# Kernel optimization log

Hardware: AMD Instinct MI355X
Metric: run time of the kernel (lower is better)

Reference implementation:

```python
import jax, jax.numpy as jnp
import numpy as np

NUM_TIMES = 1024  # times are drawn from [0, 1024), used as fixed segment count
N = 16777216


def setup_inputs() -> dict:
    key = jax.random.key(0)
    k1, k2, k3 = jax.random.split(key, 3)
    outs = jax.random.normal(k1, (N,), dtype=jnp.float32)
    T_E = jax.random.randint(k2, (N,), 0, 2, dtype=jnp.int32)
    T_T = jax.random.randint(k3, (N,), 0, NUM_TIMES, dtype=jnp.int32)
    return {"outs": outs, "T_E": T_E, "T_T": T_T}


def reference(outs, T_E, T_T):
    # E[E > 0] = 1  -> binary event indicator
    E = (T_E > 0).astype(outs.dtype)
    # Y_label_T = |T_T| ; integer times act directly as segment ids
    seg_ids = jnp.abs(T_T)
    Obs = jnp.sum(E)
    # log of running sum of hazards: log(cumsum(exp(yhat)))
    y_hat_cumsum = jnp.log(jnp.cumsum(jnp.exp(outs)))
    # original segment_max initializes accumulator at 0, so it is clipped below at 0;
    # jnp.maximum also neutralizes -inf fill for empty segments (count=0 there anyway)
    seg_max = jnp.maximum(
        jax.ops.segment_max(y_hat_cumsum, seg_ids, num_segments=NUM_TIMES), 0.0
    )
    seg_cnt = jax.ops.segment_sum(E, seg_ids, num_segments=NUM_TIMES)
    loss_s2 = jnp.sum(seg_max * seg_cnt)
    loss_s1 = jnp.sum(outs * E)
    return (loss_s2 - loss_s1) / Obs
```

## Files before the change

### kernel.cpp

```cpp
#include <hip/hip_runtime.h>

#define NUM_SEGS 1024
#define TILE_LOG 10
#define TILE (1 << TILE_LOG)
#define TPB 16
#define CHUNK (TILE * TPB)
#define BLK 256
#define NREP 32

typedef __attribute__((address_space(3))) void lds_void_t;
typedef __attribute__((address_space(1))) const void glb_void_t;

__device__ __forceinline__ void dma16(const void* g, void* l) {
    __builtin_amdgcn_global_load_lds((glb_void_t*)g, (lds_void_t*)l, 16, 0, 0);
}

__device__ __forceinline__ float waveReduceSumF(float v) {
#pragma unroll
    for (int off = 32; off > 0; off >>= 1) v += __shfl_down(v, off, 64);
    return v;
}
__device__ __forceinline__ unsigned waveReduceSumU(unsigned v) {
#pragma unroll
    for (int off = 32; off > 0; off >>= 1) v += __shfl_down(v, off, 64);
    return v;
}
__device__ __forceinline__ double waveReduceSumD(double v) {
#pragma unroll
    for (int off = 32; off > 0; off >>= 1) v += __shfl_down(v, off, 64);
    return v;
}

__global__ void init_kernel(unsigned* __restrict__ cntRep, int* __restrict__ lmaxRep,
                            unsigned* __restrict__ obs, double* __restrict__ loss1,
                            double* __restrict__ loss2, unsigned* __restrict__ counter) {
    const int t = blockIdx.x * blockDim.x + threadIdx.x;
    if (t < NREP * NUM_SEGS) { cntRep[t] = 0u; lmaxRep[t] = -1; }
    if (t == 0) { obs[0] = 0u; loss1[0] = 0.0; loss2[0] = 0.0; counter[0] = 0u; }
}

__global__ __launch_bounds__(BLK) void pass1_kernel(
    const float* __restrict__ outs, const int* __restrict__ te,
    const int* __restrict__ tt, int N,
    float* __restrict__ tile_sums, unsigned* __restrict__ cntRep,
    int* __restrict__ lmaxRep, unsigned* __restrict__ obs,
    double* __restrict__ loss1) {
    __shared__ __align__(16) float bufO[2][TILE];
    __shared__ __align__(16) int bufE[2][TILE];
    __shared__ __align__(16) int bufS[2][TILE];
    __shared__ unsigned hist[NUM_SEGS];
    __shared__ int lmax[NUM_SEGS];
    __shared__ float redF[BLK / 64];
    __shared__ float redF2[BLK / 64];
    __shared__ unsigned redU[BLK / 64];

    for (int t = threadIdx.x; t < NUM_SEGS; t += BLK) { hist[t] = 0u; lmax[t] = -1; }

    const int base = blockIdx.x * CHUNK;
    float sumOE = 0.f;
    unsigned cntE = 0u;
    const int lane = threadIdx.x & 63, wid = threadIdx.x >> 6;

    if (base + CHUNK <= N) {
        const int lofs = wid << 8;
        const int g0 = base + lofs + (lane << 2);
        auto stage = [&](int k, int b) {
            const int ge = g0 + (k << TILE_LOG);
            dma16(outs + ge, &bufO[b][lofs]);
            dma16(te + ge, &bufE[b][lofs]);
            dma16(tt + ge, &bufS[b][lofs]);
        };
        stage(0, 0);
        stage(1, 1);
        const int t4 = threadIdx.x << 2;
#pragma unroll 1
        for (int k = 0; k < TPB; ++k) {
            const int cur = k & 1;
            __syncthreads();
            const float4 o = *reinterpret_cast<const float4*>(&bufO[cur][t4]);
            const int4 ev = *reinterpret_cast<const int4*>(&bufE[cur][t4]);
            const int4 sv = *reinterpret_cast<const int4*>(&bufS[cur][t4]);
            const int gi = base + (k << TILE_LOG) + t4;
            const int s0 = sv.x < 0 ? -sv.x : sv.x;
            const int s1 = sv.y < 0 ? -sv.y : sv.y;
            const int s2 = sv.z < 0 ? -sv.z : sv.z;
            const int s3 = sv.w < 0 ? -sv.w : sv.w;
            lmax[s0] = gi;
            lmax[s1] = gi + 1;
            lmax[s2] = gi + 2;
            lmax[s3] = gi + 3;
            const float se = (__expf(o.x) + __expf(o.y)) + (__expf(o.z) + __expf(o.w));
            if (ev.x > 0) { cntE++; sumOE += o.x; atomicAdd(&hist[s0], 1u); }
            if (ev.y > 0) { cntE++; sumOE += o.y; atomicAdd(&hist[s1], 1u); }
            if (ev.z > 0) { cntE++; sumOE += o.z; atomicAdd(&hist[s2], 1u); }
            if (ev.w > 0) { cntE++; sumOE += o.w; atomicAdd(&hist[s3], 1u); }
            const float w = waveReduceSumF(se);
            if (lane == 0) redF[wid] = w;
            __syncthreads();
            if (threadIdx.x == 0)
                tile_sums[(base >> TILE_LOG) + k] =
                    (redF[0] + redF[1]) + (redF[2] + redF[3]);
            if (k + 2 < TPB) stage(k + 2, cur);
        }
    } else {
        for (int k = 0; k < TPB; ++k) {
            const int tbase = base + (k << TILE_LOG);
            float se = 0.f;
            const int end = (tbase + TILE < N) ? tbase + TILE : N;
            for (int i = tbase + (int)threadIdx.x; i < end; i += BLK) {
                const float o = outs[i];
                const int e = te[i];
                int s = tt[i]; s = s < 0 ? -s : s;
                se += __expf(o);
                lmax[s] = i;
                if (e > 0) { cntE++; sumOE += o; atomicAdd(&hist[s], 1u); }
            }
            const float w = waveReduceSumF(se);
            if (lane == 0) redF[wid] = w;
            __syncthreads();
            if (threadIdx.x == 0 && tbase < N)
                tile_sums[(base >> TILE_LOG) + k] =
                    (redF[0] + redF[1]) + (redF[2] + redF[3]);
            __syncthreads();
        }
    }
    __syncthreads();

    const int rep = (blockIdx.x & (NREP - 1)) << 10;
    for (int t = threadIdx.x; t < NUM_SEGS; t += BLK) {
        const unsigned h = hist[t];
        if (h) atomicAdd(&cntRep[rep + t], h);
        const int m = lmax[t];
        if (m >= 0) atomicMax(&lmaxRep[rep + t], m);
    }

    const float wOE = waveReduceSumF(sumOE);
    const unsigned wC = waveReduceSumU(cntE);
    if (lane == 0) { redF2[wid] = wOE; redU[wid] = wC; }
    __syncthreads();
    if (threadIdx.x == 0) {
        atomicAdd(loss1, (double)((redF2[0] + redF2[1]) + (redF2[2] + redF2[3])));
        atomicAdd(obs, redU[0] + redU[1] + redU[2] + redU[3]);
    }
}

__global__ __launch_bounds__(256) void seg_kernel(
    const float* __restrict__ outs, const float* __restrict__ tile_sums,
    const unsigned* __restrict__ cntRep, const int* __restrict__ lmaxRep,
    const double* __restrict__ loss1, double* __restrict__ loss2,
    const unsigned* __restrict__ obs, unsigned* __restrict__ counter,
    float* __restrict__ out) {
    __shared__ double redD[4];
    __shared__ unsigned redC[4];
    __shared__ int redM[4];
    const int t = blockIdx.x;
    const int lane = threadIdx.x & 63, wid = threadIdx.x >> 6;

    unsigned cnt = 0u;
    int lm = -1;
    if ((int)threadIdx.x < NREP) {
        cnt = cntRep[((int)threadIdx.x << 10) + t];
        lm = lmaxRep[((int)threadIdx.x << 10) + t];
    }
    cnt = waveReduceSumU(cnt);
#pragma unroll
    for (int off = 32; off > 0; off >>= 1) {
        const int o = __shfl_down(lm, off, 64);
        lm = lm > o ? lm : o;
    }
    if (lane == 0) { redC[wid] = cnt; redM[wid] = lm; }
    __syncthreads();
    const unsigned segcnt = redC[0] + redC[1] + redC[2] + redC[3];
    int li = redM[0] > redM[1] ? redM[0] : redM[1];
    li = li > redM[2] ? li : redM[2];
    li = li > redM[3] ? li : redM[3];

    if (li >= 0) {
        const int c = li >> TILE_LOG;
        double ps = 0.0;
        for (int j = threadIdx.x; j < c; j += 256) ps += (double)tile_sums[j];
        const int base = c << TILE_LOG;
        const int n = li - base + 1;
        const int nv = n >> 2;
        float fs = 0.f;
        if ((int)threadIdx.x < nv) {
            const float4 v =
                *reinterpret_cast<const float4*>(outs + base + ((int)threadIdx.x << 2));
            fs = (__expf(v.x) + __expf(v.y)) + (__expf(v.z) + __expf(v.w));
        }
        if ((int)threadIdx.x < (n & 3))
            fs += __expf(outs[base + (nv << 2) + (int)threadIdx.x]);
        ps += (double)fs;
        const double w = waveReduceSumD(ps);
        if (lane == 0) redD[wid] = w;
        __syncthreads();
        if (threadIdx.x == 0) {
            const double S = (redD[0] + redD[1]) + (redD[2] + redD[3]);
            double sm = log(S);
            if (sm < 0.0) sm = 0.0;
            atomicAdd(loss2, sm * (double)segcnt);
        }
    }
    __syncthreads();
    if (threadIdx.x == 0) {
        __threadfence();
        const unsigned done = atomicAdd(counter, 1u);
        if (done == gridDim.x - 1) {
            __threadfence();
            const double l2 = atomicAdd(loss2, 0.0);
            out[0] = (float)((l2 - loss1[0]) / (double)obs[0]);
        }
    }
}

extern "C" void kernel_launch(void* const* d_in, const int* in_sizes, int n_in,
                              void* d_out, int out_size, void* d_ws, size_t ws_size,
                              hipStream_t stream) {
    const float* outs = (const float*)d_in[0];
    const int* te = (const int*)d_in[1];
    const int* tt = (const int*)d_in[2];
    const int N = in_sizes[0];
    float* out = (float*)d_out;

    const int nTiles = (N + TILE - 1) >> TILE_LOG;
    const int nBlocks = (N + CHUNK - 1) / CHUNK;

    char* ws = (char*)d_ws;
    double* d_loss1 = (double*)ws;
    double* d_loss2 = d_loss1 + 1;
    unsigned* d_obs = (unsigned*)(ws + 16);
    unsigned* d_counter = d_obs + 1;
    float* d_tsums = (float*)(ws + 32);
    unsigned* d_cntRep = (unsigned*)(d_tsums + nTiles);
    int* d_lmaxRep = (int*)(d_cntRep + NREP * NUM_SEGS);

    init_kernel<<<(NREP * NUM_SEGS + 255) / 256, 256, 0, stream>>>(
        d_cntRep, d_lmaxRep, d_obs, d_loss1, d_loss2, d_counter);
    pass1_kernel<<<nBlocks, BLK, 0, stream>>>(outs, te, tt, N, d_tsums, d_cntRep,
                                              d_lmaxRep, d_obs, d_loss1);
    seg_kernel<<<NUM_SEGS, 256, 0, stream>>>(outs, d_tsums, d_cntRep, d_lmaxRep,
                                             d_loss1, d_loss2, d_obs, d_counter, out);
}
```

Before: 255.9 us.

## Split pass into stream/hist kernels and compute last-index only over tail window

Replaces the single LDS-staged pass with a register-streaming kernel for exp sums and event stats, a separate histogram kernel, and a last-occurrence kernel that only scans the final 256K elements. Segments whose last index is not in the tail fall back to a backward tile scan in seg_kernel. Adds hierarchical chunk sums to shorten prefix summation. This removes per-element LDS scatter of lmax over the whole input, at the cost of reading te twice and launching extra kernels. With uniform random times, every segment's last occurrence almost surely lands in the tail, so the fallback scan rarely runs.

```diff
diff --git a/kernel.cpp b/kernel.cpp
--- a/kernel.cpp
+++ b/kernel.cpp
@@ -3,17 +3,11 @@
 #define NUM_SEGS 1024
 #define TILE_LOG 10
 #define TILE (1 << TILE_LOG)
-#define TPB 16
-#define CHUNK (TILE * TPB)
+#define CH_LOG 13
+#define CH (1 << CH_LOG)
 #define BLK 256
 #define NREP 32
-
-typedef __attribute__((address_space(3))) void lds_void_t;
-typedef __attribute__((address_space(1))) const void glb_void_t;
-
-__device__ __forceinline__ void dma16(const void* g, void* l) {
-    __builtin_amdgcn_global_load_lds((glb_void_t*)g, (lds_void_t*)l, 16, 0, 0);
-}
+#define TAILW (1 << 18)
 
 __device__ __forceinline__ float waveReduceSumF(float v) {
 #pragma unroll
@@ -31,155 +25,191 @@
     return v;
 }
 
-__global__ void init_kernel(unsigned* __restrict__ cntRep, int* __restrict__ lmaxRep,
+__global__ void init_kernel(unsigned* __restrict__ cntRep, int* __restrict__ lmax_g,
                             unsigned* __restrict__ obs, double* __restrict__ loss1,
                             double* __restrict__ loss2, unsigned* __restrict__ counter) {
     const int t = blockIdx.x * blockDim.x + threadIdx.x;
-    if (t < NREP * NUM_SEGS) { cntRep[t] = 0u; lmaxRep[t] = -1; }
+    if (t < NREP * NUM_SEGS) cntRep[t] = 0u;
+    const int u = t - NREP * NUM_SEGS;
+    if (u >= 0 && u < NUM_SEGS) lmax_g[u] = -1;
     if (t == 0) { obs[0] = 0u; loss1[0] = 0.0; loss2[0] = 0.0; counter[0] = 0u; }
 }
 
-__global__ __launch_bounds__(BLK) void pass1_kernel(
-    const float* __restrict__ outs, const int* __restrict__ te,
-    const int* __restrict__ tt, int N,
-    float* __restrict__ tile_sums, unsigned* __restrict__ cntRep,
-    int* __restrict__ lmaxRep, unsigned* __restrict__ obs,
-    double* __restrict__ loss1) {
-    __shared__ __align__(16) float bufO[2][TILE];
-    __shared__ __align__(16) int bufE[2][TILE];
-    __shared__ __align__(16) int bufS[2][TILE];
-    __shared__ unsigned hist[NUM_SEGS];
-    __shared__ int lmax[NUM_SEGS];
-    __shared__ float redF[BLK / 64];
-    __shared__ float redF2[BLK / 64];
-    __shared__ unsigned redU[BLK / 64];
-
-    for (int t = threadIdx.x; t < NUM_SEGS; t += BLK) { hist[t] = 0u; lmax[t] = -1; }
-
-    const int base = blockIdx.x * CHUNK;
+__global__ __launch_bounds__(BLK) void stream_kernel(
+    const float* __restrict__ outs, const int* __restrict__ te, int N,
+    float* __restrict__ tile_sums, double* __restrict__ chunk_sums,
+    unsigned* __restrict__ obs, double* __restrict__ loss1) {
+    __shared__ double redD[4];
+    __shared__ float redOE[4];
+    __shared__ unsigned redU[4];
+    const int lane = threadIdx.x & 63, wid = threadIdx.x >> 6;
+    const int cbase = blockIdx.x << CH_LOG;
     float sumOE = 0.f;
     unsigned cntE = 0u;
-    const int lane = threadIdx.x & 63, wid = threadIdx.x >> 6;
-
-    if (base + CHUNK <= N) {
-        const int lofs = wid << 8;
-        const int g0 = base + lofs + (lane << 2);
-        auto stage = [&](int k, int b) {
-            const int ge = g0 + (k << TILE_LOG);
-            dma16(outs + ge, &bufO[b][lofs]);
-            dma16(te + ge, &bufE[b][lofs]);
-            dma16(tt + ge, &bufS[b][lofs]);
-        };
-        stage(0, 0);
-        stage(1, 1);
-        const int t4 = threadIdx.x << 2;
+    double chunkD = 0.0;
+
+    if (cbase + CH <= N) {
+        const float4* o4 = reinterpret_cast<const float4*>(outs);
+        const int4* e4 = reinterpret_cast<const int4*>(te);
+        const int vb = (cbase >> 2) + (wid << 9) + lane;
+        float4 oN = o4[vb];
+        int4 eN = e4[vb];
+        float ts = 0.f;
+#pragma unroll
+        for (int sub = 0; sub < 8; ++sub) {
+            const float4 oc = oN;
+            const int4 ec = eN;
+            if (sub < 7) { oN = o4[vb + (sub + 1) * 64]; eN = e4[vb + (sub + 1) * 64]; }
+            ts += (__expf(oc.x) + __expf(oc.y)) + (__expf(oc.z) + __expf(oc.w));
+            if (ec.x > 0) { cntE++; sumOE += oc.x; }
+            if (ec.y > 0) { cntE++; sumOE += oc.y; }
+            if (ec.z > 0) { cntE++; sumOE += oc.z; }
+            if (ec.w > 0) { cntE++; sumOE += oc.w; }
+            if ((sub & 3) == 3) {
+                const float w = waveReduceSumF(ts);
+                if (lane == 0) {
+                    tile_sums[(cbase >> TILE_LOG) + (wid << 1) + (sub >> 2)] = w;
+                    chunkD += (double)w;
+                }
+                ts = 0.f;
+            }
+        }
+    } else {
+        const int rbase = cbase + (wid << 11);
 #pragma unroll 1
-        for (int k = 0; k < TPB; ++k) {
-            const int cur = k & 1;
-            __syncthreads();
-            const float4 o = *reinterpret_cast<const float4*>(&bufO[cur][t4]);
-            const int4 ev = *reinterpret_cast<const int4*>(&bufE[cur][t4]);
-            const int4 sv = *reinterpret_cast<const int4*>(&bufS[cur][t4]);
-            const int gi = base + (k << TILE_LOG) + t4;
-            const int s0 = sv.x < 0 ? -sv.x : sv.x;
-            const int s1 = sv.y < 0 ? -sv.y : sv.y;
-            const int s2 = sv.z < 0 ? -sv.z : sv.z;
-            const int s3 = sv.w < 0 ? -sv.w : sv.w;
-            lmax[s0] = gi;
-            lmax[s1] = gi + 1;
-            lmax[s2] = gi + 2;
-            lmax[s3] = gi + 3;
-            const float se = (__expf(o.x) + __expf(o.y)) + (__expf(o.z) + __expf(o.w));
-            if (ev.x > 0) { cntE++; sumOE += o.x; atomicAdd(&hist[s0], 1u); }
-            if (ev.y > 0) { cntE++; sumOE += o.y; atomicAdd(&hist[s1], 1u); }
-            if (ev.z > 0) { cntE++; sumOE += o.z; atomicAdd(&hist[s2], 1u); }
-            if (ev.w > 0) { cntE++; sumOE += o.w; atomicAdd(&hist[s3], 1u); }
-            const float w = waveReduceSumF(se);
-            if (lane == 0) redF[wid] = w;
-            __syncthreads();
-            if (threadIdx.x == 0)
-                tile_sums[(base >> TILE_LOG) + k] =
-                    (redF[0] + redF[1]) + (redF[2] + redF[3]);
-            if (k + 2 < TPB) stage(k + 2, cur);
+        for (int t2 = 0; t2 < 2; ++t2) {
+            const int tbase = rbase + (t2 << TILE_LOG);
+            float ts = 0.f;
+            for (int j = 0; j < 16; ++j) {
+                const int i = tbase + j * 64 + lane;
+                if (i < N) {
+                    const float o = outs[i];
+                    ts += __expf(o);
+                    if (te[i] > 0) { cntE++; sumOE += o; }
+                }
+            }
+            const float w = waveReduceSumF(ts);
+            if (lane == 0 && tbase < N) {
+                tile_sums[tbase >> TILE_LOG] = w;
+                chunkD += (double)w;
+            }
+        }
+    }
+    if (lane == 0) { redD[wid] = chunkD; redOE[wid] = waveReduceSumF(sumOE); }
+    const float wOE = waveReduceSumF(sumOE);
+    const unsigned wC = waveReduceSumU(cntE);
+    if (lane == 0) { redOE[wid] = wOE; redU[wid] = wC; }
+    __syncthreads();
+    if (threadIdx.x == 0) {
+        chunk_sums[blockIdx.x] = (redD[0] + redD[1]) + (redD[2] + redD[3]);
+        atomicAdd(loss1, (double)((redOE[0] + redOE[1]) + (redOE[2] + redOE[3])));
+        atomicAdd(obs, redU[0] + redU[1] + redU[2] + redU[3]);
+    }
+}
+
+__global__ __launch_bounds__(BLK) void hist_kernel(
+    const int* __restrict__ te, const int* __restrict__ tt, int N,
+    unsigned* __restrict__ cntRep) {
+    __shared__ unsigned hist[NUM_SEGS];
+    for (int t = threadIdx.x; t < NUM_SEGS; t += BLK) hist[t] = 0u;
+    __syncthreads();
+    const int cbase = blockIdx.x << CH_LOG;
+    if (cbase + CH <= N) {
+        const int4* e4 = reinterpret_cast<const int4*>(te);
+        const int4* t4 = reinterpret_cast<const int4*>(tt);
+        const int vb = (cbase >> 2) + (int)threadIdx.x;
+        int4 eN = e4[vb], tN = t4[vb];
+#pragma unroll
+        for (int j = 0; j < CH / (BLK * 4); ++j) {
+            const int4 ec = eN, tc = tN;
+            if (j + 1 < CH / (BLK * 4)) {
+                eN = e4[vb + (j + 1) * BLK];
+                tN = t4[vb + (j + 1) * BLK];
+            }
+            if (ec.x > 0) atomicAdd(&hist[tc.x < 0 ? -tc.x : tc.x], 1u);
+            if (ec.y > 0) atomicAdd(&hist[tc.y < 0 ? -tc.y : tc.y], 1u);
+            if (ec.z > 0) atomicAdd(&hist[tc.z < 0 ? -tc.z : tc.z], 1u);
+            if (ec.w > 0) atomicAdd(&hist[tc.w < 0 ? -tc.w : tc.w], 1u);
         }
     } else {
-        for (int k = 0; k < TPB; ++k) {
-            const int tbase = base + (k << TILE_LOG);
-            float se = 0.f;
-            const int end = (tbase + TILE < N) ? tbase + TILE : N;
-            for (int i = tbase + (int)threadIdx.x; i < end; i += BLK) {
-                const float o = outs[i];
-                const int e = te[i];
-                int s = tt[i]; s = s < 0 ? -s : s;
-                se += __expf(o);
-                lmax[s] = i;
-                if (e > 0) { cntE++; sumOE += o; atomicAdd(&hist[s], 1u); }
-            }
-            const float w = waveReduceSumF(se);
-            if (lane == 0) redF[wid] = w;
-            __syncthreads();
-            if (threadIdx.x == 0 && tbase < N)
-                tile_sums[(base >> TILE_LOG) + k] =
-                    (redF[0] + redF[1]) + (redF[2] + redF[3]);
-            __syncthreads();
-        }
-    }
-    __syncthreads();
-
+        for (int i = cbase + (int)threadIdx.x; i < N; i += BLK) {
+            if (te[i] > 0) { int s = tt[i]; s = s < 0 ? -s : s; atomicAdd(&hist[s], 1u); }
+        }
+    }
+    __syncthreads();
     const int rep = (blockIdx.x & (NREP - 1)) << 10;
     for (int t = threadIdx.x; t < NUM_SEGS; t += BLK) {
         const unsigned h = hist[t];
         if (h) atomicAdd(&cntRep[rep + t], h);
+    }
+}
+
+__global__ __launch_bounds__(BLK) void taillmax_kernel(
+    const int* __restrict__ tt, int N, int tailStart, int* __restrict__ lmax_g) {
+    __shared__ int lmax[NUM_SEGS];
+    for (int t = threadIdx.x; t < NUM_SEGS; t += BLK) lmax[t] = -1;
+    __syncthreads();
+    const int cbase = tailStart + (blockIdx.x << CH_LOG);
+    const int end = (cbase + CH < N) ? cbase + CH : N;
+    for (int i = cbase + (int)threadIdx.x; i < end; i += BLK) {
+        int s = tt[i]; s = s < 0 ? -s : s;
+        lmax[s] = i;
+    }
+    __syncthreads();
+    for (int t = threadIdx.x; t < NUM_SEGS; t += BLK) {
         const int m = lmax[t];
-        if (m >= 0) atomicMax(&lmaxRep[rep + t], m);
-    }
-
-    const float wOE = waveReduceSumF(sumOE);
-    const unsigned wC = waveReduceSumU(cntE);
-    if (lane == 0) { redF2[wid] = wOE; redU[wid] = wC; }
-    __syncthreads();
-    if (threadIdx.x == 0) {
-        atomicAdd(loss1, (double)((redF2[0] + redF2[1]) + (redF2[2] + redF2[3])));
-        atomicAdd(obs, redU[0] + redU[1] + redU[2] + redU[3]);
+        if (m >= 0) atomicMax(&lmax_g[t], m);
     }
 }
 
 __global__ __launch_bounds__(256) void seg_kernel(
-    const float* __restrict__ outs, const float* __restrict__ tile_sums,
-    const unsigned* __restrict__ cntRep, const int* __restrict__ lmaxRep,
+    const float* __restrict__ outs, const int* __restrict__ tt,
+    const float* __restrict__ tile_sums, const double* __restrict__ chunk_sums,
+    const unsigned* __restrict__ cntRep, const int* __restrict__ lmax_g, int N,
     const double* __restrict__ loss1, double* __restrict__ loss2,
     const unsigned* __restrict__ obs, unsigned* __restrict__ counter,
     float* __restrict__ out) {
     __shared__ double redD[4];
     __shared__ unsigned redC[4];
-    __shared__ int redM[4];
+    __shared__ int sMax;
     const int t = blockIdx.x;
     const int lane = threadIdx.x & 63, wid = threadIdx.x >> 6;
 
     unsigned cnt = 0u;
-    int lm = -1;
-    if ((int)threadIdx.x < NREP) {
-        cnt = cntRep[((int)threadIdx.x << 10) + t];
-        lm = lmaxRep[((int)threadIdx.x << 10) + t];
-    }
+    if ((int)threadIdx.x < NREP) cnt = cntRep[((int)threadIdx.x << 10) + t];
     cnt = waveReduceSumU(cnt);
-#pragma unroll
-    for (int off = 32; off > 0; off >>= 1) {
-        const int o = __shfl_down(lm, off, 64);
-        lm = lm > o ? lm : o;
-    }
-    if (lane == 0) { redC[wid] = cnt; redM[wid] = lm; }
+    if (lane == 0) redC[wid] = cnt;
     __syncthreads();
     const unsigned segcnt = redC[0] + redC[1] + redC[2] + redC[3];
-    int li = redM[0] > redM[1] ? redM[0] : redM[1];
-    li = li > redM[2] ? li : redM[2];
-    li = li > redM[3] ? li : redM[3];
-
-    if (li >= 0) {
-        const int c = li >> TILE_LOG;
+
+    if (segcnt > 0) {
+        int li = lmax_g[t];
+        if (li < 0) {
+            if (threadIdx.x == 0) sMax = -1;
+            __syncthreads();
+            for (int base = ((N - 1) >> TILE_LOG) << TILE_LOG;
+                 base >= 0; base -= TILE) {
+                int loc = -1;
+                const int end = (base + TILE < N) ? base + TILE : N;
+                for (int j = base + (int)threadIdx.x; j < end; j += 256) {
+                    int s = tt[j]; s = s < 0 ? -s : s;
+                    if (s == t && j > loc) loc = j;
+                }
+                if (loc >= 0) atomicMax(&sMax, loc);
+                __syncthreads();
+                if (sMax >= 0) break;
+                __syncthreads();
+            }
+            li = sMax;
+        }
+        const int cchunk = li >> CH_LOG;
+        const int ctile = li >> TILE_LOG;
         double ps = 0.0;
-        for (int j = threadIdx.x; j < c; j += 256) ps += (double)tile_sums[j];
-        const int base = c << TILE_LOG;
+        for (int j = threadIdx.x; j < cchunk; j += 256) ps += chunk_sums[j];
+        for (int j = (cchunk << (CH_LOG - TILE_LOG)) + (int)threadIdx.x; j < ctile;
+             j += 256)
+            ps += (double)tile_sums[j];
+        const int base = ctile << TILE_LOG;
         const int n = li - base + 1;
         const int nv = n >> 2;
         float fs = 0.f;
@@ -222,22 +252,28 @@
     const int N = in_sizes[0];
     float* out = (float*)d_out;
 
+    const int nCh = (N + CH - 1) >> CH_LOG;
     const int nTiles = (N + TILE - 1) >> TILE_LOG;
-    const int nBlocks = (N + CHUNK - 1) / CHUNK;
+    const int tailStart = (N > TAILW) ? N - TAILW : 0;
+    const int nBt = (N - tailStart + CH - 1) >> CH_LOG;
 
     char* ws = (char*)d_ws;
     double* d_loss1 = (double*)ws;
     double* d_loss2 = d_loss1 + 1;
     unsigned* d_obs = (unsigned*)(ws + 16);
     unsigned* d_counter = d_obs + 1;
-    float* d_tsums = (float*)(ws + 32);
+    double* d_csums = (double*)(ws + 32);
+    float* d_tsums = (float*)(d_csums + nCh);
     unsigned* d_cntRep = (unsigned*)(d_tsums + nTiles);
-    int* d_lmaxRep = (int*)(d_cntRep + NREP * NUM_SEGS);
-
-    init_kernel<<<(NREP * NUM_SEGS + 255) / 256, 256, 0, stream>>>(
-        d_cntRep, d_lmaxRep, d_obs, d_loss1, d_loss2, d_counter);
-    pass1_kernel<<<nBlocks, BLK, 0, stream>>>(outs, te, tt, N, d_tsums, d_cntRep,
-                                              d_lmaxRep, d_obs, d_loss1);
-    seg_kernel<<<NUM_SEGS, 256, 0, stream>>>(outs, d_tsums, d_cntRep, d_lmaxRep,
-                                             d_loss1, d_loss2, d_obs, d_counter, out);
-}
+    int* d_lmax = (int*)(d_cntRep + NREP * NUM_SEGS);
+
+    init_kernel<<<(NREP * NUM_SEGS + NUM_SEGS + 255) / 256, 256, 0, stream>>>(
+        d_cntRep, d_lmax, d_obs, d_loss1, d_loss2, d_counter);
+    stream_kernel<<<nCh, BLK, 0, stream>>>(outs, te, N, d_tsums, d_csums, d_obs,
+                                           d_loss1);
+    hist_kernel<<<nCh, BLK, 0, stream>>>(te, tt, N, d_cntRep);
+    taillmax_kernel<<<nBt, BLK, 0, stream>>>(tt, N, tailStart, d_lmax);
+    seg_kernel<<<NUM_SEGS, 256, 0, stream>>>(outs, tt, d_tsums, d_csums, d_cntRep,
+                                             d_lmax, N, d_loss1, d_loss2, d_obs,
+                                             d_counter, out);
+}
```

Measured after the change: 253.9 us. About the same (-0.8%).
